# Kernel tuning notes

Measured on AMD Instinct MI355X. Metric: run time of the kernel, lower is better.

The kernel has to match this reference:

```python
import jax, jax.numpy as jnp
import numpy as np

N_NODES = 10000
N_EDGES = 320000
D_FEAT = 128


def setup_inputs() -> dict:
    key = jax.random.key(0)
    k1, k2, k3 = jax.random.split(key, 3)
    node_states = jax.random.normal(k1, (N_NODES, D_FEAT), dtype=jnp.float32)
    edge_sources = jax.random.randint(k2, (N_EDGES,), 0, N_NODES, dtype=jnp.int32).astype(jnp.int64)
    edge_targets = jax.random.randint(k3, (N_EDGES,), 0, N_NODES, dtype=jnp.int32).astype(jnp.int64)
    return {"node_states": node_states, "edge_sources": edge_sources, "edge_targets": edge_targets}


def reference(node_states, edge_sources, edge_targets):
    # Original torch code computes one_hot(edge_sources) @ node_states, which is
    # mathematically an index-gather of node rows per edge. We implement the
    # equivalent gather directly (same math, no O(E*N) wasted GEMM work).
    msg_from_source = jnp.take(node_states, edge_sources, axis=0)  # [E, D]
    msg_from_target = jnp.take(node_states, edge_targets, axis=0)  # [E, D]
    node_msgs = jnp.concatenate([msg_from_source, msg_from_target], axis=-1)  # [E, 2D]
    return node_msgs
```

## Files before the change

### kernel.cpp

```cpp
#include <hip/hip_runtime.h>


typedef float v4f __attribute__((ext_vector_type(4)));

#define EPW 8

__global__ __launch_bounds__(256) void NodePropagator_75110388073048_kernel(
    const v4f* __restrict__ ns,
    const int* __restrict__ src32,
    const int* __restrict__ tgt32,
    v4f* __restrict__ out,
    int nEdges)
{
    int tid  = blockIdx.x * blockDim.x + threadIdx.x;
    int wid  = tid >> 6;
    int lane = tid & 63;
    int half = lane >> 5;
    int c    = lane & 31;

    int e0 = wid * EPW;
    if (e0 >= nEdges) return;

    bool is_i64 = (src32[1] == 0) & (src32[3] == 0) &
                  (src32[5] == 0) & (src32[7] == 0);
    int stride = is_i64 ? 2 : 1;

    const int* idxp = half ? tgt32 : src32;

    int rows[EPW];
#pragma unroll
    for (int k = 0; k < EPW; ++k) {
        int e  = e0 + k;
        int ec = e < nEdges ? e : nEdges - 1;
        rows[k] = idxp[ec * stride];
    }

    v4f v[EPW];
#pragma unroll
    for (int k = 0; k < EPW; ++k)
        v[k] = ns[rows[k] * 32 + c];

#pragma unroll
    for (int k = 0; k < EPW; ++k) {
        int e = e0 + k;
        if (e < nEdges)
            __builtin_nontemporal_store(v[k], &out[e * 64 + lane]);
    }
}

extern "C" void kernel_launch(void* const* d_in, const int* in_sizes, int n_in,
                              void* d_out, int out_size, void* d_ws, size_t ws_size,
                              hipStream_t stream) {
    const v4f* ns  = (const v4f*)d_in[0];
    const int* src = (const int*)d_in[1];
    const int* tgt = (const int*)d_in[2];
    v4f*       out = (v4f*)d_out;

    int nEdges = in_sizes[1];
    long long waves  = ((long long)nEdges + EPW - 1) / EPW;
    long long threads = waves * 64;
    int block = 256;
    int grid  = (int)((threads + block - 1) / block);

    NodePropagator_75110388073048_kernel<<<grid, block, 0, stream>>>(
        ns, src, tgt, out, nEdges);
}
```

Before: 334.1 us.

## Split gather by node-row halves across interleaved block groups for cache locality

Launches each edge group twice, once for source rows below a fixed split and once for rows above it. Blocks are interleaved so adjacent blocks handle different halves. The aim is to give each XCD or L2 slice a smaller working set of node rows and raise cache hit rates. In exchange, every block reads the index arrays twice, runs twice as many waves, and issues partial, divergent stores. The split point is hardcoded to half the test node count.

```diff
diff --git a/kernel.cpp b/kernel.cpp
--- a/kernel.cpp
+++ b/kernel.cpp
@@ -4,22 +4,27 @@
 typedef float v4f __attribute__((ext_vector_type(4)));
 
 #define EPW 8
+#define ROW_SPLIT 5000
 
 __global__ __launch_bounds__(256) void NodePropagator_75110388073048_kernel(
     const v4f* __restrict__ ns,
     const int* __restrict__ src32,
     const int* __restrict__ tgt32,
     v4f* __restrict__ out,
-    int nEdges)
+    int nEdges, int nGroups)
 {
-    int tid  = blockIdx.x * blockDim.x + threadIdx.x;
-    int wid  = tid >> 6;
-    int lane = tid & 63;
+    int lane = threadIdx.x & 63;
+    int wIn  = threadIdx.x >> 6;
+    int b    = blockIdx.x;
+
+    int side     = (b & 7) >> 2;
+    int idxInGrp = (b >> 3) * 4 + (b & 3);
+    int wg       = idxInGrp * 4 + wIn;
+    if (wg >= nGroups) return;
+    int e0 = wg * EPW;
+
     int half = lane >> 5;
     int c    = lane & 31;
-
-    int e0 = wid * EPW;
-    if (e0 >= nEdges) return;
 
     bool is_i64 = (src32[1] == 0) & (src32[3] == 0) &
                   (src32[5] == 0) & (src32[7] == 0);
@@ -28,22 +33,25 @@
     const int* idxp = half ? tgt32 : src32;
 
     int rows[EPW];
+    bool own[EPW];
 #pragma unroll
     for (int k = 0; k < EPW; ++k) {
-        int e  = e0 + k;
-        int ec = e < nEdges ? e : nEdges - 1;
-        rows[k] = idxp[ec * stride];
+        int e = e0 + k;
+        if (e >= nEdges) e = nEdges - 1;
+        rows[k] = idxp[e * stride];
+        own[k] = (rows[k] < ROW_SPLIT) == (side == 0);
     }
 
     v4f v[EPW];
 #pragma unroll
-    for (int k = 0; k < EPW; ++k)
-        v[k] = ns[rows[k] * 32 + c];
+    for (int k = 0; k < EPW; ++k) {
+        if (own[k]) v[k] = ns[rows[k] * 32 + c];
+    }
 
 #pragma unroll
     for (int k = 0; k < EPW; ++k) {
         int e = e0 + k;
-        if (e < nEdges)
+        if (own[k] && e < nEdges)
             __builtin_nontemporal_store(v[k], &out[e * 64 + lane]);
     }
 }
@@ -56,12 +64,14 @@
     const int* tgt = (const int*)d_in[2];
     v4f*       out = (v4f*)d_out;
 
-    int nEdges = in_sizes[1];
-    long long waves  = ((long long)nEdges + EPW - 1) / EPW;
-    long long threads = waves * 64;
+    int nEdges  = in_sizes[1];
+    int nGroups = (nEdges + EPW - 1) / EPW;
+
     int block = 256;
-    int grid  = (int)((threads + block - 1) / block);
+    int blocksPerSide = (nGroups + 3) / 4;
+    int oct  = (blocksPerSide + 3) / 4;
+    int grid = oct * 8;
 
     NodePropagator_75110388073048_kernel<<<grid, block, 0, stream>>>(
-        ns, src, tgt, out, nEdges);
+        ns, src, tgt, out, nEdges, nGroups);
 }
```

New measurement: 417.0 us. +24.8%, slower.
